# Kernel optimization log

Measured on AMD Instinct MI355X. Metric: run time of the kernel, lower is better.

Reference implementation:

```python
import jax, jax.numpy as jnp
import numpy as np

D_MODEL = 768; N_LAYER = 4; D_STATE = 64; D_CONV = 4; EXPAND = 2; HEADDIM = 64
D_INNER = EXPAND * D_MODEL          # 1536
NHEADS = D_INNER // HEADDIM         # 24
CONV_DIM = D_INNER + 2 * D_STATE    # 1664
D_IN_PROJ = 2 * D_INNER + 2 * D_STATE + NHEADS  # 3224
VOCAB = 50257; EPS = 1e-5


def _ln(x, w, b):
    m = x.mean(-1, keepdims=True)
    v = ((x - m) ** 2).mean(-1, keepdims=True)
    return (x - m) * jax.lax.rsqrt(v + EPS) * w + b


def _silu(x):
    return x * jax.nn.sigmoid(x)


def _mamba2(x, W_in, conv_w, conv_b, dt_bias, A_log, Dp, rms_w, W_out):
    # x: [B, L, d_model]
    Bsz, L, _ = x.shape
    zxbcdt = x @ W_in.T                                   # [B,L,D_IN_PROJ]
    z = zxbcdt[..., :D_INNER]
    xBC = zxbcdt[..., D_INNER:D_INNER + CONV_DIM]
    dt = zxbcdt[..., D_INNER + CONV_DIM:]                 # [B,L,H]
    # causal depthwise conv over time
    xc = jnp.transpose(xBC, (0, 2, 1))                    # [B,C,L]
    xc = jax.lax.conv_general_dilated(
        xc, conv_w[:, None, :], (1,), [(D_CONV - 1, 0)],
        dimension_numbers=('NCH', 'OIH', 'NCH'), feature_group_count=CONV_DIM)
    xBC = _silu(jnp.transpose(xc, (0, 2, 1)) + conv_b)
    xh = xBC[..., :D_INNER].reshape(Bsz, L, NHEADS, HEADDIM)
    Bc = xBC[..., D_INNER:D_INNER + D_STATE]              # [B,L,N]
    Cc = xBC[..., D_INNER + D_STATE:]                     # [B,L,N]
    dt = jax.nn.softplus(dt + dt_bias)                    # [B,L,H]
    dA = jnp.exp(dt * (-jnp.exp(A_log)))                  # [B,L,H]

    def step(h, inp):
        dA_t, dt_t, x_t, B_t, C_t = inp
        h = dA_t[:, :, None, None] * h + (dt_t[:, :, None] * x_t)[..., None] * B_t[:, None, None, :]
        return h, jnp.einsum('bhpn,bn->bhp', h, C_t)

    tm = lambda a: jnp.moveaxis(a, 1, 0)  # time-major
    h0 = jnp.zeros((Bsz, NHEADS, HEADDIM, D_STATE), x.dtype)
    _, y = jax.lax.scan(step, h0, (tm(dA), tm(dt), tm(xh), tm(Bc), tm(Cc)))
    y = jnp.moveaxis(y, 0, 1) + Dp[:, None] * xh          # [B,L,H,P]
    y = y.reshape(Bsz, L, D_INNER) * _silu(z)             # gate
    y = y * jax.lax.rsqrt((y * y).mean(-1, keepdims=True) + EPS) * rms_w
    return y @ W_out.T


def setup_inputs() -> dict:
    key = jax.random.key(0)
    ks = jax.random.split(key, 16)
    B, L = 1, 1024
    idx = jax.random.randint(ks[0], (B, L), 0, VOCAB)
    targets = jax.random.randint(ks[1], (B, L), 0, VOCAB)
    s = 0.02
    emb = jax.random.normal(ks[2], (VOCAB, D_MODEL), jnp.float32) * s
    ln_w = jnp.ones((N_LAYER, D_MODEL)); ln_b = jnp.zeros((N_LAYER, D_MODEL))
    W_in = jax.random.normal(ks[3], (N_LAYER, D_IN_PROJ, D_MODEL), jnp.float32) * s
    conv_w = jax.random.normal(ks[4], (N_LAYER, CONV_DIM, D_CONV), jnp.float32) * 0.1
    conv_b = jnp.zeros((N_LAYER, CONV_DIM))
    dt_bias = jnp.log(jnp.expm1(jax.random.uniform(ks[5], (N_LAYER, NHEADS), minval=0.001, maxval=0.1)))
    A_log = jnp.log(jax.random.uniform(ks[6], (N_LAYER, NHEADS), minval=1.0, maxval=16.0))
    Dp = jnp.ones((N_LAYER, NHEADS))
    rms_w = jnp.ones((N_LAYER, D_INNER))
    W_out = jax.random.normal(ks[7], (N_LAYER, D_MODEL, D_INNER), jnp.float32) * s
    lnf_w = jnp.ones((D_MODEL,)); lnf_b = jnp.zeros((D_MODEL,))
    return {"idx": idx, "targets": targets, "emb": emb, "ln_w": ln_w, "ln_b": ln_b,
            "W_in": W_in, "conv_w": conv_w, "conv_b": conv_b, "dt_bias": dt_bias,
            "A_log": A_log, "Dp": Dp, "rms_w": rms_w, "W_out": W_out,
            "lnf_w": lnf_w, "lnf_b": lnf_b}


def reference(idx, targets, emb, ln_w, ln_b, W_in, conv_w, conv_b, dt_bias,
              A_log, Dp, rms_w, W_out, lnf_w, lnf_b):
    x = emb[idx]                                          # [B,L,D]
    for i in range(N_LAYER):
        x = x + _mamba2(_ln(x, ln_w[i], ln_b[i]), W_in[i], conv_w[i], conv_b[i],
                        dt_bias[i], A_log[i], Dp[i], rms_w[i], W_out[i])
    x = _ln(x, lnf_w, lnf_b)
    logits = x @ emb.T                                    # tied head
    logp = jax.nn.log_softmax(logits, axis=-1)
    loss = -jnp.take_along_axis(logp, targets[..., None], axis=-1).mean()
    return logits, loss
```

## Files before the change

kernel.cpp:

```cpp
#include <hip/hip_runtime.h>
#include <hip/hip_bf16.h>
#include <math.h>

#define SL     1024
#define DMODEL 768
#define NLAYER 4
#define NSTATE 64
#define HEADDIM 64
#define DINNER 1536
#define NHEADS 24
#define CONVDIM 1664
#define DINPROJ 3224
#define VOCABN 50257

typedef __attribute__((ext_vector_type(8))) short short8;
typedef __attribute__((ext_vector_type(4))) short short4v;
typedef __attribute__((ext_vector_type(4))) float f32x4;

__device__ __forceinline__ short f2bf(float f) {
    unsigned int u = __builtin_bit_cast(unsigned int, f);
    u += 0x7fffu + ((u >> 16) & 1u);
    return (short)(u >> 16);
}

#define AS1 __attribute__((address_space(1)))
#define AS3 __attribute__((address_space(3)))
__device__ __forceinline__ void gl2lds16(const void* g, void* l) {
    __builtin_amdgcn_global_load_lds((const AS1 unsigned int*)g,
                                     (AS3 unsigned int*)(unsigned int)(uintptr_t)l,
                                     16, 0, 0);
}

template <int CTRL>
__device__ __forceinline__ float dppadd(float x) {
    int v = __builtin_amdgcn_update_dpp(0, __builtin_bit_cast(int, x), CTRL, 0xf, 0xf, true);
    return x + __builtin_bit_cast(float, v);
}

__global__ void cvt_k(const float* __restrict__ s, short* __restrict__ d, int n) {
    int i = (blockIdx.x * 256 + threadIdx.x) * 4;
    if (i >= n) return;
    float4 v = *(const float4*)(s + i);
    short4v o;
    o.x = f2bf(v.x); o.y = f2bf(v.y); o.z = f2bf(v.z); o.w = f2bf(v.w);
    *(short4v*)(d + i) = o;
}

__global__ void embed_k(const int* __restrict__ idx, const float* __restrict__ emb,
                        float* __restrict__ x) {
    int d = blockIdx.x * 256 + threadIdx.x;
    int t = blockIdx.y;
    x[t * DMODEL + d] = emb[(size_t)idx[t] * DMODEL + d];
}

__global__ void ln_k(const float* __restrict__ x, const float* __restrict__ w,
                     const float* __restrict__ b, short* __restrict__ out) {
    int row = blockIdx.x, t = threadIdx.x;
    const float* xr = x + row * DMODEL;
    float v0 = xr[t], v1 = xr[t + 256], v2 = xr[t + 512];
    float s = v0 + v1 + v2;
    float q = v0 * v0 + v1 * v1 + v2 * v2;
    __shared__ float sa[4], sb[4];
    for (int off = 32; off; off >>= 1) { s += __shfl_down(s, off); q += __shfl_down(q, off); }
    if (!(t & 63)) { sa[t >> 6] = s; sb[t >> 6] = q; }
    __syncthreads();
    s = sa[0] + sa[1] + sa[2] + sa[3];
    q = sb[0] + sb[1] + sb[2] + sb[3];
    float mean = s * (1.f / DMODEL);
    float var  = q * (1.f / DMODEL) - mean * mean;
    float rs = rsqrtf(var + 1e-5f);
    out[row * DMODEL + t      ] = f2bf((v0 - mean) * rs * w[t      ] + b[t      ]);
    out[row * DMODEL + t + 256] = f2bf((v1 - mean) * rs * w[t + 256] + b[t + 256]);
    out[row * DMODEL + t + 512] = f2bf((v2 - mean) * rs * w[t + 512] + b[t + 512]);
}

__global__ __launch_bounds__(512) void gemm_bb_k(const short* __restrict__ A,
                                                 const short* __restrict__ B,
                                                 float* __restrict__ C,
                                                 float2* __restrict__ P,
                                                 int N, int K, int addflag) {
    __shared__ __align__(16) short As[2][16384];
    __shared__ __align__(16) short Bs[2][16384];
    const int t = threadIdx.x;
    const int lane = t & 63, wv = t >> 6;

    const int nwg = gridDim.x;
    int bid = blockIdx.x;
    int qq = nwg >> 3, rr = nwg & 7;
    int xcd = bid & 7, ii = bid >> 3;
    int v = (xcd < rr ? xcd * (qq + 1) : rr * (qq + 1) + (xcd - rr) * qq) + ii;
    const int m0 = (v & 3) * 256;
    const int n0 = (v >> 2) * 256;

    const int wm = (wv >> 2) * 128, wn = (wv & 3) * 64;
    const int q4 = lane >> 4, l16 = lane & 15;

    f32x4 zero4 = {0.f, 0.f, 0.f, 0.f};
    f32x4 acc[8][4];
#pragma unroll
    for (int i = 0; i < 8; i++)
#pragma unroll
        for (int j = 0; j < 4; j++) acc[i][j] = zero4;

    auto stage = [&](int buf, int k0) {
#pragma unroll
        for (int i = 0; i < 4; i++) {
            int g = i * 512 + t;
            int q = g >> 8, r = g & 255;
            gl2lds16(A + (size_t)(m0 + r) * K + k0 + q * 8, &As[buf][g * 8]);
        }
#pragma unroll
        for (int i = 0; i < 4; i++) {
            int g = i * 512 + t;
            int q = g >> 8, r = g & 255;
            int gr = n0 + r; if (gr > N - 1) gr = N - 1;
            gl2lds16(B + (size_t)gr * K + k0 + q * 8, &Bs[buf][g * 8]);
        }
    };

    const int NT = K >> 6;
    stage(0, 0);
    for (int tt = 0; tt < NT; tt++) {
        const int cur = tt & 1;
        if (tt + 1 < NT) {
            stage(cur ^ 1, (tt + 1) << 6);
            asm volatile("s_waitcnt vmcnt(8)" ::: "memory");
        } else {
            asm volatile("s_waitcnt vmcnt(0)" ::: "memory");
        }
        __builtin_amdgcn_s_barrier();

#pragma unroll
        for (int kk = 0; kk < 2; kk++) {
            short8 af[8], bf[4];
#pragma unroll
            for (int nt = 0; nt < 4; nt++)
                bf[nt] = *(const short8*)(&Bs[cur][(kk * 4 + q4) * 2048 + (wn + nt * 16 + l16) * 8]);
#pragma unroll
            for (int mt = 0; mt < 8; mt++)
                af[mt] = *(const short8*)(&As[cur][(kk * 4 + q4) * 2048 + (wm + mt * 16 + l16) * 8]);
#pragma unroll
            for (int mt = 0; mt < 8; mt++)
#pragma unroll
                for (int nt = 0; nt < 4; nt++)
                    acc[mt][nt] = __builtin_amdgcn_mfma_f32_16x16x32_bf16(af[mt], bf[nt], acc[mt][nt], 0, 0, 0);
        }
        asm volatile("s_waitcnt lgkmcnt(0)" ::: "memory");
        __builtin_amdgcn_s_barrier();
    }

#pragma unroll
    for (int mt = 0; mt < 8; mt++) {
        int row = m0 + wm + mt * 16 + q4 * 4;
#pragma unroll
        for (int nt = 0; nt < 4; nt++) {
            int col = n0 + wn + nt * 16 + l16;
            if (col < N) {
#pragma unroll
                for (int r = 0; r < 4; r++) {
                    size_t o = (size_t)(row + r) * N + col;
                    float val = acc[mt][nt][r];
                    if (addflag) C[o] += val; else C[o] = val;
                }
            }
        }
    }

    float2* lds_ms = (float2*)&As[0][0];
    const int nw = wv & 3;
#pragma unroll
    for (int mt = 0; mt < 8; mt++) {
#pragma unroll
        for (int r = 0; r < 4; r++) {
            float m = -3.0e38f;
#pragma unroll
            for (int nt = 0; nt < 4; nt++) {
                int col = n0 + wn + nt * 16 + l16;
                if (col < N) m = fmaxf(m, acc[mt][nt][r]);
            }
#pragma unroll
            for (int off = 1; off < 16; off <<= 1)
                m = fmaxf(m, __shfl_xor(m, off));
            float s = 0.f;
#pragma unroll
            for (int nt = 0; nt < 4; nt++) {
                int col = n0 + wn + nt * 16 + l16;
                if (col < N) s += __expf(acc[mt][nt][r] - m);
            }
#pragma unroll
            for (int off = 1; off < 16; off <<= 1)
                s += __shfl_xor(s, off);
            if (l16 == 0)
                lds_ms[(wm + mt * 16 + q4 * 4 + r) * 5 + nw] = make_float2(m, s);
        }
    }
    __syncthreads();
    if (t < 256) {
        float m = -3.0e38f, s = 0.f;
#pragma unroll
        for (int w = 0; w < 4; w++) {
            float2 p = lds_ms[t * 5 + w];
            float nm = fmaxf(m, p.x);
            s = s * __expf(m - nm) + p.y * __expf(p.x - nm);
            m = nm;
        }
        P[(size_t)(v >> 2) * 1024 + (m0 + t)] = make_float2(m, s);
    }
}

__global__ __launch_bounds__(256) void gemm64_k(const short* __restrict__ A,
                                                const short* __restrict__ B,
                                                float* __restrict__ C,
                                                int N, int K, int addflag, int nMB) {
    __shared__ __align__(16) short As[2][4096];
    __shared__ __align__(16) short Bs[2][4096];
    const int t = threadIdx.x;
    const int lane = t & 63, wv = t >> 6;

    const int nwg = gridDim.x;
    int bid = blockIdx.x;
    int qq = nwg >> 3, rr = nwg & 7;
    int xcd = bid & 7, ii = bid >> 3;
    int v = (xcd < rr ? xcd * (qq + 1) : rr * (qq + 1) + (xcd - rr) * qq) + ii;
    const int m0 = (v % nMB) * 64, n0 = (v / nMB) * 64;

    const int wm = (wv >> 1) * 32, wn = (wv & 1) * 32;
    const int q4 = lane >> 4, l16 = lane & 15;

    f32x4 zero4 = {0.f, 0.f, 0.f, 0.f};
    f32x4 acc[2][2];
#pragma unroll
    for (int i = 0; i < 2; i++)
#pragma unroll
        for (int j = 0; j < 2; j++) acc[i][j] = zero4;

    auto stage = [&](int buf, int k0) {
#pragma unroll
        for (int i = 0; i < 2; i++) {
            int g = i * 256 + t;
            int q = g >> 6, r = g & 63;
            gl2lds16(A + (size_t)(m0 + r) * K + k0 + q * 8, &As[buf][g * 8]);
        }
#pragma unroll
        for (int i = 0; i < 2; i++) {
            int g = i * 256 + t;
            int q = g >> 6, r = g & 63;
            int gr = n0 + r; if (gr > N - 1) gr = N - 1;
            gl2lds16(B + (size_t)gr * K + k0 + q * 8, &Bs[buf][g * 8]);
        }
    };

    const int NT = K >> 6;
    stage(0, 0);
    for (int tt = 0; tt < NT; tt++) {
        const int cur = tt & 1;
        if (tt + 1 < NT) {
            stage(cur ^ 1, (tt + 1) << 6);
            asm volatile("s_waitcnt vmcnt(4)" ::: "memory");
        } else {
            asm volatile("s_waitcnt vmcnt(0)" ::: "memory");
        }
        __builtin_amdgcn_s_barrier();

        short8 af[2][2], bf[2][2];
#pragma unroll
        for (int kk = 0; kk < 2; kk++) {
#pragma unroll
            for (int mt = 0; mt < 2; mt++)
                af[kk][mt] = *(const short8*)(&As[cur][(kk * 4 + q4) * 512 + (wm + mt * 16 + l16) * 8]);
#pragma unroll
            for (int nt = 0; nt < 2; nt++)
                bf[kk][nt] = *(const short8*)(&Bs[cur][(kk * 4 + q4) * 512 + (wn + nt * 16 + l16) * 8]);
        }
        asm volatile("s_waitcnt lgkmcnt(0)" ::: "memory");
        __builtin_amdgcn_s_barrier();

#pragma unroll
        for (int kk = 0; kk < 2; kk++)
#pragma unroll
            for (int mt = 0; mt < 2; mt++)
#pragma unroll
                for (int nt = 0; nt < 2; nt++)
                    acc[mt][nt] = __builtin_amdgcn_mfma_f32_16x16x32_bf16(af[kk][mt], bf[kk][nt], acc[mt][nt], 0, 0, 0);
    }

#pragma unroll
    for (int mt = 0; mt < 2; mt++) {
        int row = m0 + wm + mt * 16 + (lane >> 4) * 4;
#pragma unroll
        for (int nt = 0; nt < 2; nt++) {
            int col = n0 + wn + nt * 16 + l16;
            if (col < N) {
#pragma unroll
                for (int r = 0; r < 4; r++) {
                    size_t o = (size_t)(row + r) * N + col;
                    float val = acc[mt][nt][r];
                    if (addflag) C[o] += val; else C[o] = val;
                }
            }
        }
    }
}

#define LDSK 56
__global__ __launch_bounds__(256) void gemm_bt_k(const short* __restrict__ A,
                                                 const float* __restrict__ B,
                                                 float* __restrict__ C,
                                                 int N, int K, int addflag) {
    __shared__ __align__(16) short As[128 * LDSK];
    __shared__ __align__(16) short Bs[128 * LDSK];
    const int t = threadIdx.x;
    const int lane = t & 63, wv = t >> 6;
    const int m0 = blockIdx.x * 128, n0 = blockIdx.y * 128;
    const int wm = (wv >> 1) * 64, wn = (wv & 1) * 64;
    f32x4 zero4 = {0.f, 0.f, 0.f, 0.f};
    f32x4 acc[4][4];
#pragma unroll
    for (int i = 0; i < 4; i++)
#pragma unroll
        for (int j = 0; j < 4; j++) acc[i][j] = zero4;
    for (int k0 = 0; k0 < K; k0 += 32) {
        uint4  av[2];
        float4 bv[4];
#pragma unroll
        for (int i = 0; i < 2; i++) {
            int c = i * 256 + t, row = c >> 2, kc = c & 3;
            av[i] = *(const uint4*)(A + (size_t)(m0 + row) * K + k0 + kc * 8);
        }
#pragma unroll
        for (int i = 0; i < 4; i++) {
            int c = i * 256 + t, row = c >> 3, kc = c & 7;
            int gr = n0 + row; if (gr > N - 1) gr = N - 1;
            bv[i] = *(const float4*)(B + (size_t)gr * K + k0 + kc * 4);
        }
        __syncthreads();
#pragma unroll
        for (int i = 0; i < 2; i++) {
            int c = i * 256 + t, row = c >> 2, kc = c & 3;
            *(uint4*)(As + row * LDSK + kc * 8) = av[i];
        }
#pragma unroll
        for (int i = 0; i < 4; i++) {
            int c = i * 256 + t, row = c >> 3, kc = c & 7;
            short4v sv;
            sv.x = f2bf(bv[i].x); sv.y = f2bf(bv[i].y);
            sv.z = f2bf(bv[i].z); sv.w = f2bf(bv[i].w);
            *(short4v*)(Bs + row * LDSK + kc * 4) = sv;
        }
        __syncthreads();
        short8 af[4], bf[4];
#pragma unroll
        for (int mt = 0; mt < 4; mt++)
            af[mt] = *(const short8*)(As + (wm + mt * 16 + (lane & 15)) * LDSK + (lane >> 4) * 8);
#pragma unroll
        for (int nt = 0; nt < 4; nt++)
            bf[nt] = *(const short8*)(Bs + (wn + nt * 16 + (lane & 15)) * LDSK + (lane >> 4) * 8);
#pragma unroll
        for (int mt = 0; mt < 4; mt++)
#pragma unroll
            for (int nt = 0; nt < 4; nt++)
                acc[mt][nt] = __builtin_amdgcn_mfma_f32_16x16x32_bf16(af[mt], bf[nt], acc[mt][nt], 0, 0, 0);
    }
#pragma unroll
    for (int mt = 0; mt < 4; mt++) {
        int row = m0 + wm + mt * 16 + (lane >> 4) * 4;
#pragma unroll
        for (int nt = 0; nt < 4; nt++) {
            int col = n0 + wn + nt * 16 + (lane & 15);
            if (col < N) {
#pragma unroll
                for (int r = 0; r < 4; r++) {
                    size_t o = (size_t)(row + r) * N + col;
                    float val = acc[mt][nt][r];
                    if (addflag) C[o] += val; else C[o] = val;
                }
            }
        }
    }
}

__global__ void convdt_k(const float* __restrict__ zx, const float* __restrict__ cw,
                         const float* __restrict__ cb, const float* __restrict__ dt_bias,
                         const float* __restrict__ A_log, float* __restrict__ xbc,
                         float* __restrict__ dts, float* __restrict__ dAv) {
    int c = blockIdx.x * 256 + threadIdx.x;
    int t = blockIdx.y;
    if (c < CONVDIM) {
        float acc = cb[c];
#pragma unroll
        for (int j = 0; j < 4; j++) {
            int ts = t - 3 + j;
            if (ts >= 0) acc += cw[c * 4 + j] * zx[(size_t)ts * DINPROJ + DINNER + c];
        }
        xbc[(size_t)t * CONVDIM + c] = acc / (1.f + __expf(-acc));
    } else if (c < CONVDIM + NHEADS) {
        int h = c - CONVDIM;
        float d = zx[(size_t)t * DINPROJ + 3200 + h] + dt_bias[h];
        float sp = (d > 20.f) ? d : log1pf(__expf(d));
        dts[t * NHEADS + h] = sp;
        dAv[t * NHEADS + h] = __expf(-__expf(A_log[h]) * sp);
    }
}

__global__ __launch_bounds__(128) void scan_k(const float* __restrict__ xbc,
                                              const float* __restrict__ dts,
                                              const float* __restrict__ dAv,
                                              float* __restrict__ yraw) {
    __shared__ __align__(16) float BCs[64][128];
    __shared__ __align__(16) float xs[64][8];
    __shared__ float dash[64];
    int h = blockIdx.x >> 3;
    int pbase = (blockIdx.x & 7) * 8;
    int t = threadIdx.x, lane = t & 63, wv = t >> 6;
    int pl = wv * 4 + (lane >> 4);
    int n4 = lane & 15;
    float s0 = 0.f, s1 = 0.f, s2 = 0.f, s3 = 0.f;

    for (int tc = 0; tc < 16; tc++) {
        __syncthreads();
#pragma unroll 4
        for (int it = 0; it < 16; it++) {
            int idx = it * 128 + t;
            int trow = idx >> 5, c4 = idx & 31;
            *(float4*)&BCs[trow][c4 * 4] =
                *(const float4*)(xbc + (size_t)(tc * 64 + trow) * CONVDIM + DINNER + c4 * 4);
        }
        {
            int trow = t >> 1, hf = t & 1;
            float dtv = dts[(tc * 64 + trow) * NHEADS + h];
            float4 xv = *(const float4*)(xbc + (size_t)(tc * 64 + trow) * CONVDIM
                                         + h * HEADDIM + pbase + hf * 4);
            xv.x *= dtv; xv.y *= dtv; xv.z *= dtv; xv.w *= dtv;
            *(float4*)&xs[trow][hf * 4] = xv;
        }
        if (t < 64) dash[t] = dAv[(tc * 64 + t) * NHEADS + h];
        __syncthreads();

#pragma unroll 4
        for (int tt = 0; tt < 64; tt++) {
            float4 B4 = *(const float4*)&BCs[tt][n4 * 4];
            float4 C4 = *(const float4*)&BCs[tt][64 + n4 * 4];
            float dtx = xs[tt][pl];
            float da = dash[tt];
            s0 = fmaf(da, s0, dtx * B4.x);
            s1 = fmaf(da, s1, dtx * B4.y);
            s2 = fmaf(da, s2, dtx * B4.z);
            s3 = fmaf(da, s3, dtx * B4.w);
            float part = s0 * C4.x;
            part = fmaf(s1, C4.y, part);
            part = fmaf(s2, C4.z, part);
            part = fmaf(s3, C4.w, part);
            part = dppadd<0xB1>(part);
            part = dppadd<0x4E>(part);
            part = dppadd<0x114>(part);
            part = dppadd<0x118>(part);
            if (n4 == 0)
                yraw[(size_t)(tc * 64 + tt) * DINNER + h * HEADDIM + pbase + pl] = part;
        }
    }
}

__global__ void rms_k(const float* __restrict__ yraw, const float* __restrict__ zx,
                      const float* __restrict__ xbc, const float* __restrict__ Dp,
                      const float* __restrict__ rw, short* __restrict__ yn) {
    int row = blockIdx.x, t = threadIdx.x;
    float v[6];
    float q = 0.f;
#pragma unroll
    for (int j = 0; j < 6; j++) {
        int i = t + j * 256;
        float z  = zx[(size_t)row * DINPROJ + i];
        float xh = xbc[(size_t)row * CONVDIM + i];
        float y  = yraw[(size_t)row * DINNER + i] + Dp[i >> 6] * xh;
        float val = y * (z / (1.f + __expf(-z)));
        v[j] = val;
        q += val * val;
    }
    __shared__ float sb[4];
    for (int off = 32; off; off >>= 1) q += __shfl_down(q, off);
    if (!(t & 63)) sb[t >> 6] = q;
    __syncthreads();
    q = sb[0] + sb[1] + sb[2] + sb[3];
    float rs = rsqrtf(q * (1.f / DINNER) + 1e-5f);
#pragma unroll
    for (int j = 0; j < 6; j++) {
        int i = t + j * 256;
        yn[(size_t)row * DINNER + i] = f2bf(v[j] * rs * rw[i]);
    }
}

__global__ void loss_row_k(const float* __restrict__ logits, const int* __restrict__ tg,
                           float* __restrict__ lossp) {
    int r = blockIdx.x, t = threadIdx.x;
    const float* lr = logits + (size_t)r * VOCABN;
    float m = -3.0e38f, s = 0.f;
    for (int j = t; j < VOCABN; j += 256) {
        float v = lr[j];
        if (v > m) { s = s * __expf(m - v) + 1.f; m = v; }
        else s += __expf(v - m);
    }
    for (int off = 32; off; off >>= 1) {
        float mo = __shfl_down(m, off), so = __shfl_down(s, off);
        float nm = fmaxf(m, mo);
        s = s * __expf(m - nm) + so * __expf(mo - nm);
        m = nm;
    }
    __shared__ float sm[4], ss[4];
    if (!(t & 63)) { sm[t >> 6] = m; ss[t >> 6] = s; }
    __syncthreads();
    if (t == 0) {
        m = sm[0]; s = ss[0];
        for (int w = 1; w < 4; w++) {
            float nm = fmaxf(m, sm[w]);
            s = s * __expf(m - nm) + ss[w] * __expf(sm[w] - nm);
            m = nm;
        }
        lossp[r] = (m + logf(s)) - lr[tg[r]];
    }
}

__global__ void loss_fin2_k(const float2* __restrict__ P, const float* __restrict__ logits,
                            const int* __restrict__ tg, float* __restrict__ lossp) {
    int r = blockIdx.x * 256 + threadIdx.x;
    float m = -3.0e38f, s = 0.f;
    for (int p = 0; p < 197; p++) {
        float2 q = P[(size_t)p * 1024 + r];
        float nm = fmaxf(m, q.x);
        s = s * __expf(m - nm) + q.y * __expf(q.x - nm);
        m = nm;
    }
    lossp[r] = (m + logf(s)) - logits[(size_t)r * VOCABN + tg[r]];
}

__global__ void loss_fin_k(const float* __restrict__ lossp, float* __restrict__ out) {
    int t = threadIdx.x;
    float s = lossp[t] + lossp[t + 256] + lossp[t + 512] + lossp[t + 768];
    for (int off = 32; off; off >>= 1) s += __shfl_down(s, off);
    __shared__ float sb[4];
    if (!(t & 63)) sb[t >> 6] = s;
    __syncthreads();
    if (t == 0) out[(size_t)SL * VOCABN] = (sb[0] + sb[1] + sb[2] + sb[3]) * (1.f / SL);
}

extern "C" void kernel_launch(void* const* d_in, const int* in_sizes, int n_in,
                              void* d_out, int out_size, void* d_ws, size_t ws_size,
                              hipStream_t stream) {
    const int*   idx     = (const int*)d_in[0];
    const int*   targets = (const int*)d_in[1];
    const float* emb     = (const float*)d_in[2];
    const float* ln_w    = (const float*)d_in[3];
    const float* ln_b    = (const float*)d_in[4];
    const float* W_in    = (const float*)d_in[5];
    const float* conv_w  = (const float*)d_in[6];
    const float* conv_b  = (const float*)d_in[7];
    const float* dt_bias = (const float*)d_in[8];
    const float* A_log   = (const float*)d_in[9];
    const float* Dp      = (const float*)d_in[10];
    const float* rms_w   = (const float*)d_in[11];
    const float* W_out   = (const float*)d_in[12];
    const float* lnf_w   = (const float*)d_in[13];
    const float* lnf_b   = (const float*)d_in[14];

    char* ws = (char*)d_ws;
    float* x     = (float*)(ws + 0);
    short* xn    = (short*)(ws + 3145728);
    float* zx    = (float*)(ws + 4718592);
    float* xbc   = (float*)(ws + 17924096);
    float* dts   = (float*)(ws + 24739840);
    float* dAv   = (float*)(ws + 24838144);
    float* yraw  = (float*)(ws + 24936448);
    short* yn    = (short*)(ws + 31227904);
    float* lossp = (float*)(ws + 34373632);
    short* wInb  = (short*)(ws + 34377728);
    short* wOutb = (short*)(ws + 54183936);
    short* embb  = (short*)(ws + 63621120);
    float2* pms  = (float2*)(ws + 4718592);
    float* logits = (float*)d_out;

    const bool big = ws_size >= 140815872ull;

    if (big) {
        int nWin  = NLAYER * DINPROJ * DMODEL;
        int nWout = NLAYER * DMODEL * DINNER;
        int nEmb  = VOCABN * DMODEL;
        cvt_k<<<(nWin / 4 + 255) / 256, 256, 0, stream>>>(W_in, wInb, nWin);
        cvt_k<<<(nWout / 4 + 255) / 256, 256, 0, stream>>>(W_out, wOutb, nWout);
        cvt_k<<<(nEmb / 4 + 255) / 256, 256, 0, stream>>>(emb, embb, nEmb);
    }

    embed_k<<<dim3(3, SL), 256, 0, stream>>>(idx, emb, x);
    for (int l = 0; l < NLAYER; l++) {
        ln_k<<<SL, 256, 0, stream>>>(x, ln_w + l * DMODEL, ln_b + l * DMODEL, xn);
        if (big)
            gemm64_k<<<816, 256, 0, stream>>>(xn, wInb + (size_t)l * DINPROJ * DMODEL,
                                              zx, DINPROJ, DMODEL, 0, 16);
        else
            gemm_bt_k<<<dim3(8, 26), 256, 0, stream>>>(xn, W_in + (size_t)l * DINPROJ * DMODEL,
                                                       zx, DINPROJ, DMODEL, 0);
        convdt_k<<<dim3(7, SL), 256, 0, stream>>>(zx, conv_w + l * CONVDIM * 4,
                                                  conv_b + l * CONVDIM,
                                                  dt_bias + l * NHEADS, A_log + l * NHEADS,
                                                  xbc, dts, dAv);
        scan_k<<<192, 128, 0, stream>>>(xbc, dts, dAv, yraw);
        rms_k<<<SL, 256, 0, stream>>>(yraw, zx, xbc, Dp + l * NHEADS, rms_w + l * DINNER, yn);
        if (big)
            gemm64_k<<<192, 256, 0, stream>>>(yn, wOutb + (size_t)l * DMODEL * DINNER,
                                              x, DMODEL, DINNER, 1, 16);
        else
            gemm_bt_k<<<dim3(8, 6), 256, 0, stream>>>(yn, W_out + (size_t)l * DMODEL * DINNER,
                                                      x, DMODEL, DINNER, 1);
    }
    ln_k<<<SL, 256, 0, stream>>>(x, lnf_w, lnf_b, xn);
    if (big) {
        gemm_bb_k<<<4 * 197, 512, 0, stream>>>(xn, embb, logits, pms, VOCABN, DMODEL, 0);
        loss_fin2_k<<<4, 256, 0, stream>>>(pms, logits, targets, lossp);
    } else {
        gemm_bt_k<<<dim3(8, 393), 256, 0, stream>>>(xn, emb, logits, VOCABN, DMODEL, 0);
        loss_row_k<<<SL, 256, 0, stream>>>(logits, targets, lossp);
    }
    loss_fin_k<<<1, 256, 0, stream>>>(lossp, logits);
}
```

Baseline: 1.149 ms.

## Split GEMM k-tile into four phases interleaving prefetch with MFMA and setprio

Restructures the 256x256 bf16 GEMM main loop into four sub-phases, each separated by barriers. Each phase reads LDS fragments, issues part of the next tile's global-to-LDS loads (A in phase one, B in phase two), then runs MFMAs at raised wave priority. The shared-memory layout is reorganised into 128-row halves so each wave reads a contiguous region. The goal is to overlap global loads with compute and keep the matrix units busy, at the cost of many more barriers and a full vmcnt(0) wait at the top of each iteration.

```diff
diff --git a/kernel.cpp b/kernel.cpp
--- a/kernel.cpp
+++ b/kernel.cpp
@@ -94,6 +94,8 @@
 
     const int wm = (wv >> 2) * 128, wn = (wv & 3) * 64;
     const int q4 = lane >> 4, l16 = lane & 15;
+    const int abase = (wm >> 7) * 8192;
+    const int bbase = (wn >> 7) * 8192 + (wn & 64) * 8;
 
     f32x4 zero4 = {0.f, 0.f, 0.f, 0.f};
     f32x4 acc[8][4];
@@ -102,51 +104,108 @@
 #pragma unroll
         for (int j = 0; j < 4; j++) acc[i][j] = zero4;
 
-    auto stage = [&](int buf, int k0) {
-#pragma unroll
-        for (int i = 0; i < 4; i++) {
+    auto stageA = [&](int buf, int half, int k0) {
+#pragma unroll
+        for (int i = 0; i < 2; i++) {
             int g = i * 512 + t;
-            int q = g >> 8, r = g & 255;
-            gl2lds16(A + (size_t)(m0 + r) * K + k0 + q * 8, &As[buf][g * 8]);
-        }
-#pragma unroll
-        for (int i = 0; i < 4; i++) {
+            int q = g >> 7, rh = g & 127;
+            gl2lds16(A + (size_t)(m0 + half * 128 + rh) * K + k0 + q * 8,
+                     &As[buf][half * 8192 + g * 8]);
+        }
+    };
+    auto stageB = [&](int buf, int half, int k0) {
+#pragma unroll
+        for (int i = 0; i < 2; i++) {
             int g = i * 512 + t;
-            int q = g >> 8, r = g & 255;
-            int gr = n0 + r; if (gr > N - 1) gr = N - 1;
-            gl2lds16(B + (size_t)gr * K + k0 + q * 8, &Bs[buf][g * 8]);
+            int q = g >> 7, rh = g & 127;
+            int gr = n0 + half * 128 + rh; if (gr > N - 1) gr = N - 1;
+            gl2lds16(B + (size_t)gr * K + k0 + q * 8,
+                     &Bs[buf][half * 8192 + g * 8]);
         }
     };
 
     const int NT = K >> 6;
-    stage(0, 0);
+    stageA(0, 0, 0); stageA(0, 1, 0); stageB(0, 0, 0); stageB(0, 1, 0);
+
     for (int tt = 0; tt < NT; tt++) {
         const int cur = tt & 1;
-        if (tt + 1 < NT) {
-            stage(cur ^ 1, (tt + 1) << 6);
-            asm volatile("s_waitcnt vmcnt(8)" ::: "memory");
-        } else {
-            asm volatile("s_waitcnt vmcnt(0)" ::: "memory");
-        }
+        const bool pf = (tt + 1 < NT);
+        const int k1 = (tt + 1) << 6;
+        const short* Ac = &As[cur][abase];
+        const short* Bc = &Bs[cur][bbase];
+
+        asm volatile("s_waitcnt vmcnt(0)" ::: "memory");
         __builtin_amdgcn_s_barrier();
 
-#pragma unroll
-        for (int kk = 0; kk < 2; kk++) {
-            short8 af[8], bf[4];
+        short8 bfk[4];
+        {
+            short8 af[4];
 #pragma unroll
             for (int nt = 0; nt < 4; nt++)
-                bf[nt] = *(const short8*)(&Bs[cur][(kk * 4 + q4) * 2048 + (wn + nt * 16 + l16) * 8]);
-#pragma unroll
-            for (int mt = 0; mt < 8; mt++)
-                af[mt] = *(const short8*)(&As[cur][(kk * 4 + q4) * 2048 + (wm + mt * 16 + l16) * 8]);
-#pragma unroll
-            for (int mt = 0; mt < 8; mt++)
+                bfk[nt] = *(const short8*)(Bc + q4 * 1024 + (nt * 16 + l16) * 8);
+#pragma unroll
+            for (int mt = 0; mt < 4; mt++)
+                af[mt] = *(const short8*)(Ac + q4 * 1024 + (mt * 16 + l16) * 8);
+            if (pf) { stageA(cur ^ 1, 0, k1); stageA(cur ^ 1, 1, k1); }
+            __builtin_amdgcn_s_barrier();
+            __builtin_amdgcn_s_setprio(1);
+#pragma unroll
+            for (int mt = 0; mt < 4; mt++)
 #pragma unroll
                 for (int nt = 0; nt < 4; nt++)
-                    acc[mt][nt] = __builtin_amdgcn_mfma_f32_16x16x32_bf16(af[mt], bf[nt], acc[mt][nt], 0, 0, 0);
-        }
-        asm volatile("s_waitcnt lgkmcnt(0)" ::: "memory");
-        __builtin_amdgcn_s_barrier();
+                    acc[mt][nt] = __builtin_amdgcn_mfma_f32_16x16x32_bf16(af[mt], bfk[nt], acc[mt][nt], 0, 0, 0);
+            __builtin_amdgcn_s_setprio(0);
+            __builtin_amdgcn_s_barrier();
+        }
+        {
+            short8 af[4];
+#pragma unroll
+            for (int mt = 0; mt < 4; mt++)
+                af[mt] = *(const short8*)(Ac + q4 * 1024 + ((mt + 4) * 16 + l16) * 8);
+            if (pf) { stageB(cur ^ 1, 0, k1); stageB(cur ^ 1, 1, k1); }
+            __builtin_amdgcn_s_barrier();
+            __builtin_amdgcn_s_setprio(1);
+#pragma unroll
+            for (int mt = 0; mt < 4; mt++)
+#pragma unroll
+                for (int nt = 0; nt < 4; nt++)
+                    acc[mt + 4][nt] = __builtin_amdgcn_mfma_f32_16x16x32_bf16(af[mt], bfk[nt], acc[mt + 4][nt], 0, 0, 0);
+            __builtin_amdgcn_s_setprio(0);
+            __builtin_amdgcn_s_barrier();
+        }
+        {
+            short8 af[4];
+#pragma unroll
+            for (int nt = 0; nt < 4; nt++)
+                bfk[nt] = *(const short8*)(Bc + (4 + q4) * 1024 + (nt * 16 + l16) * 8);
+#pragma unroll
+            for (int mt = 0; mt < 4; mt++)
+                af[mt] = *(const short8*)(Ac + (4 + q4) * 1024 + (mt * 16 + l16) * 8);
+            __builtin_amdgcn_s_barrier();
+            __builtin_amdgcn_s_setprio(1);
+#pragma unroll
+            for (int mt = 0; mt < 4; mt++)
+#pragma unroll
+                for (int nt = 0; nt < 4; nt++)
+                    acc[mt][nt] = __builtin_amdgcn_mfma_f32_16x16x32_bf16(af[mt], bfk[nt], acc[mt][nt], 0, 0, 0);
+            __builtin_amdgcn_s_setprio(0);
+            __builtin_amdgcn_s_barrier();
+        }
+        {
+            short8 af[4];
+#pragma unroll
+            for (int mt = 0; mt < 4; mt++)
+                af[mt] = *(const short8*)(Ac + (4 + q4) * 1024 + ((mt + 4) * 16 + l16) * 8);
+            __builtin_amdgcn_s_barrier();
+            __builtin_amdgcn_s_setprio(1);
+#pragma unroll
+            for (int mt = 0; mt < 4; mt++)
+#pragma unroll
+                for (int nt = 0; nt < 4; nt++)
+                    acc[mt + 4][nt] = __builtin_amdgcn_mfma_f32_16x16x32_bf16(af[mt], bfk[nt], acc[mt + 4][nt], 0, 0, 0);
+            __builtin_amdgcn_s_setprio(0);
+            __builtin_amdgcn_s_barrier();
+        }
     }
 
 #pragma unroll
```

Measured after the change: 1.129 ms. No clear change (-1.8%).
